# Optimization experiments

Hardware: AMD Instinct MI355X
Metric: run time of the kernel (lower is better)

Reference implementation:

```python
import jax, jax.numpy as jnp
import numpy as np

DIM = 1024
DIM_HEAD = 64
HEADS = 16
INNER = DIM_HEAD * HEADS  # 1024
B, N1, N2 = 8, 4096, 256
EPS = 1e-5


def layer_norm(x, w, b):
    mu = jnp.mean(x, axis=-1, keepdims=True)
    var = jnp.var(x, axis=-1, keepdims=True)
    return (x - mu) * jax.lax.rsqrt(var + EPS) * w + b


def setup_inputs() -> dict:
    key = jax.random.key(0)
    ks = jax.random.split(key, 10)
    return {
        "x": jax.random.normal(ks[0], (B, N1, DIM), jnp.float32),
        "latents": jax.random.normal(ks[1], (B, N2, DIM), jnp.float32),
        "shift": jax.random.normal(ks[2], (B, DIM), jnp.float32),
        "scale": jax.random.normal(ks[3], (B, DIM), jnp.float32),
        "ln1_w": jnp.ones((DIM,), jnp.float32),
        "ln1_b": jnp.zeros((DIM,), jnp.float32),
        "ln2_w": jnp.ones((DIM,), jnp.float32),
        "ln2_b": jnp.zeros((DIM,), jnp.float32),
        "Wq": jax.random.normal(ks[4], (INNER, DIM), jnp.float32) * 0.02,
        "Wkv": jax.random.normal(ks[5], (2 * INNER, DIM), jnp.float32) * 0.02,
        "Wo": jax.random.normal(ks[6], (DIM, INNER), jnp.float32) * 0.02,
    }


def reference(x, latents, shift, scale, ln1_w, ln1_b, ln2_w, ln2_b, Wq, Wkv, Wo):
    x = layer_norm(x, ln1_w, ln1_b)                      # (b, n1, D)
    lat = layer_norm(latents, ln2_w, ln2_b)              # (b, n2, D)
    lat = lat * (1.0 + scale[:, None, :]) + shift[:, None, :]

    b, n2, _ = lat.shape
    q = jnp.einsum('bld,ed->ble', lat, Wq)               # (b, n2, inner)
    kv_in = jnp.concatenate((x, lat), axis=-2)           # (b, n1+n2, D)
    kv = jnp.einsum('bld,ed->ble', kv_in, Wkv)           # (b, n1+n2, 2*inner)
    k, v = jnp.split(kv, 2, axis=-1)

    def to_heads(t):
        bsz, L, _ = t.shape
        return t.reshape(bsz, L, HEADS, DIM_HEAD).transpose(0, 2, 1, 3)

    q, k, v = to_heads(q), to_heads(k), to_heads(v)      # (b, h, L, dh)
    attn_scale = 1.0 / np.sqrt(np.sqrt(DIM_HEAD)).astype(np.float32)
    logits = jnp.einsum('bhqd,bhkd->bhqk', q * attn_scale, k * attn_scale)
    w = jax.nn.softmax(logits.astype(jnp.float32), axis=-1).astype(logits.dtype)
    out = jnp.einsum('bhqk,bhkd->bhqd', w, v)            # (b, h, n2, dh)
    out = out.transpose(0, 2, 1, 3).reshape(b, n2, INNER)
    return jnp.einsum('ble,de->bld', out, Wo)            # (b, n2, D)
```

## Files before the change

### kernel.cpp

```cpp
#include <hip/hip_runtime.h>
#include <cstdint>
#include <cstddef>

#define B_SZ 8
#define N1 4096
#define N2 256
#define LTOT 4352
#define DIMD 1024
#define HEADS 16
#define DH 64
#define MKV (B_SZ * LTOT)

typedef _Float16 f16;
typedef f16 f16x4_t __attribute__((ext_vector_type(4)));
typedef f16 f16x8_t __attribute__((ext_vector_type(8)));
typedef float f32x4_t __attribute__((ext_vector_type(4)));

__device__ __forceinline__ void g2l16(const void* g, void* l) {
  __builtin_amdgcn_global_load_lds(
      (__attribute__((address_space(1))) void*)g,
      (__attribute__((address_space(3))) void*)l, 16, 0, 0);
}

__global__ __launch_bounds__(256) void ln_mod_kernel(
    const float* __restrict__ x, const float* __restrict__ lat,
    const float* __restrict__ shift, const float* __restrict__ scale,
    const float* __restrict__ ln1w, const float* __restrict__ ln1b,
    const float* __restrict__ ln2w, const float* __restrict__ ln2b,
    f16* __restrict__ kv_in) {
  const int row = blockIdx.x;
  const int b = row / LTOT;
  const int n = row - b * LTOT;
  const int tid = threadIdx.x;
  const bool is_lat = (n >= N1);
  const float* src = is_lat ? (lat + (size_t)(b * N2 + (n - N1)) * DIMD)
                            : (x + (size_t)(b * N1 + n) * DIMD);
  float4 v = ((const float4*)src)[tid];
  float s = v.x + v.y + v.z + v.w;
  float s2 = v.x * v.x + v.y * v.y + v.z * v.z + v.w * v.w;
#pragma unroll
  for (int m = 1; m <= 32; m <<= 1) {
    s += __shfl_xor(s, m, 64);
    s2 += __shfl_xor(s2, m, 64);
  }
  __shared__ float red[8];
  const int wave = tid >> 6;
  if ((tid & 63) == 0) { red[wave * 2] = s; red[wave * 2 + 1] = s2; }
  __syncthreads();
  s = red[0] + red[2] + red[4] + red[6];
  s2 = red[1] + red[3] + red[5] + red[7];
  const float mean = s * (1.0f / DIMD);
  const float var = fmaxf(s2 * (1.0f / DIMD) - mean * mean, 0.0f);
  const float rstd = rsqrtf(var + 1e-5f);
  const float4 w4 = ((const float4*)(is_lat ? ln2w : ln1w))[tid];
  const float4 b4 = ((const float4*)(is_lat ? ln2b : ln1b))[tid];
  float y0 = (v.x - mean) * rstd * w4.x + b4.x;
  float y1 = (v.y - mean) * rstd * w4.y + b4.y;
  float y2 = (v.z - mean) * rstd * w4.z + b4.z;
  float y3 = (v.w - mean) * rstd * w4.w + b4.w;
  if (is_lat) {
    float4 sc = ((const float4*)(scale + (size_t)b * DIMD))[tid];
    float4 sh = ((const float4*)(shift + (size_t)b * DIMD))[tid];
    y0 = y0 * (1.0f + sc.x) + sh.x;
    y1 = y1 * (1.0f + sc.y) + sh.y;
    y2 = y2 * (1.0f + sc.z) + sh.z;
    y3 = y3 * (1.0f + sc.w) + sh.w;
  }
  f16x4_t o = {(f16)y0, (f16)y1, (f16)y2, (f16)y3};
  *(f16x4_t*)(kv_in + (size_t)row * DIMD + tid * 4) = o;
}

__global__ __launch_bounds__(256) void cast_kernel(const float* __restrict__ in,
                                                   f16* __restrict__ out, int n4) {
  const int i = blockIdx.x * 256 + threadIdx.x;
  if (i < n4) {
    float4 v = ((const float4*)in)[i];
    f16x4_t o = {(f16)v.x, (f16)v.y, (f16)v.z, (f16)v.w};
    ((f16x4_t*)out)[i] = o;
  }
}

template <int MODE>
__global__ __launch_bounds__(256) void gemm128(
    const f16* __restrict__ A0, const f16* __restrict__ BT,
    void* __restrict__ out0, void* __restrict__ out1) {
  const int mt = blockIdx.x, nt = blockIdx.y;
  const f16* Abase;
  if (MODE == 1) {
    const int bb = mt >> 1;
    Abase = A0 + ((size_t)(bb * LTOT + N1 + (mt & 1) * 128)) * DIMD;
  } else {
    Abase = A0 + (size_t)mt * 128 * DIMD;
  }
  const f16* Bbase = BT + (size_t)nt * 128 * DIMD;
  __shared__ alignas(16) f16 As[128 * 32];
  __shared__ alignas(16) f16 Bs[128 * 32];
  const int tid = threadIdx.x;
  const int wave = tid >> 6, lane = tid & 63;
  const int wm = (wave & 1) * 64, wn = (wave >> 1) * 64;
  const int lrow = lane >> 2, lcol = (lane & 3) * 8;
  const int r16 = lane & 15, g8 = (lane >> 4) * 8, q4 = (lane >> 4) * 4;
  f32x4_t acc[4][4] = {};
  for (int k0 = 0; k0 < DIMD; k0 += 32) {
    __syncthreads();
    g2l16(Abase + (size_t)(wave * 16 + lrow) * DIMD + k0 + lcol, &As[(wave * 16) * 32]);
    g2l16(Abase + (size_t)(64 + wave * 16 + lrow) * DIMD + k0 + lcol, &As[(64 + wave * 16) * 32]);
    g2l16(Bbase + (size_t)(wave * 16 + lrow) * DIMD + k0 + lcol, &Bs[(wave * 16) * 32]);
    g2l16(Bbase + (size_t)(64 + wave * 16 + lrow) * DIMD + k0 + lcol, &Bs[(64 + wave * 16) * 32]);
    __syncthreads();
    f16x8_t a[4], bf[4];
#pragma unroll
    for (int i = 0; i < 4; i++)
      a[i] = *(const f16x8_t*)&As[(wm + i * 16 + r16) * 32 + g8];
#pragma unroll
    for (int j = 0; j < 4; j++)
      bf[j] = *(const f16x8_t*)&Bs[(wn + j * 16 + r16) * 32 + g8];
#pragma unroll
    for (int i = 0; i < 4; i++)
#pragma unroll
      for (int j = 0; j < 4; j++)
        acc[i][j] = __builtin_amdgcn_mfma_f32_16x16x32_f16(a[i], bf[j], acc[i][j], 0, 0, 0);
  }

  if constexpr (MODE == 0) {
    const int m0 = mt * 128;
    const int b = m0 / LTOT;
    const int n0 = m0 - b * LTOT;
    const int e0 = nt * 128;
    if (e0 < 1024) {
      f16* kbuf = (f16*)out0;
#pragma unroll
      for (int i = 0; i < 4; i++) {
        const int n_base = n0 + wm + i * 16 + q4;
#pragma unroll
        for (int j = 0; j < 4; j++) {
          const int e = e0 + wn + j * 16 + r16;
          const int h = e >> 6, d = e & 63;
          const size_t base = ((size_t)(b * HEADS + h) * LTOT);
#pragma unroll
          for (int r = 0; r < 4; r++)
            kbuf[(base + n_base + r) * DH + d] = (f16)acc[i][j][r];
        }
      }
    } else {
      f16* vbuf = (f16*)out1;
      const int e0v = e0 - 1024;
#pragma unroll
      for (int i = 0; i < 4; i++) {
        const int n_base = n0 + wm + i * 16 + q4;
#pragma unroll
        for (int j = 0; j < 4; j++) {
          const int e = e0v + wn + j * 16 + r16;
          const int h = e >> 6, d = e & 63;
          f16x4_t pk = {(f16)acc[i][j][0], (f16)acc[i][j][1],
                        (f16)acc[i][j][2], (f16)acc[i][j][3]};
          *(f16x4_t*)&vbuf[((size_t)(b * HEADS + h) * DH + d) * LTOT + n_base] = pk;
        }
      }
    }
  } else if constexpr (MODE == 1) {
    f16* qbuf = (f16*)out0;
    const int b = mt >> 1;
#pragma unroll
    for (int i = 0; i < 4; i++) {
      const int n_base = (mt & 1) * 128 + wm + i * 16 + q4;
#pragma unroll
      for (int j = 0; j < 4; j++) {
        const int e = nt * 128 + wn + j * 16 + r16;
        const int h = e >> 6, d = e & 63;
#pragma unroll
        for (int r = 0; r < 4; r++)
          qbuf[((size_t)(b * HEADS + h) * N2 + n_base + r) * DH + d] = (f16)acc[i][j][r];
      }
    }
  } else {
    float* outp = (float*)out0;
    const int m0 = mt * 128;
#pragma unroll
    for (int i = 0; i < 4; i++) {
#pragma unroll
      for (int j = 0; j < 4; j++) {
        const int col = nt * 128 + wn + j * 16 + r16;
#pragma unroll
        for (int r = 0; r < 4; r++)
          outp[(size_t)(m0 + wm + i * 16 + q4 + r) * DIMD + col] = acc[i][j][r];
      }
    }
  }
}

__global__ __launch_bounds__(256, 1) void attn_kernel(
    const f16* __restrict__ qbuf, const f16* __restrict__ kbuf,
    const f16* __restrict__ vbuf, f16* __restrict__ attn_out) {
  const int bh = blockIdx.x >> 1;
  const int qt = blockIdx.x & 1;
  const int b = bh >> 4, h = bh & 15;
  const f16* qg = qbuf + ((size_t)bh * N2 + qt * 128) * DH;
  const f16* kg = kbuf + (size_t)bh * LTOT * DH;
  const f16* vg = vbuf + (size_t)bh * DH * LTOT;

  __shared__ alignas(16) f16 Rh[17408];
  __shared__ alignas(16) f16 Vs[4][64 * 32];

  const int tid = threadIdx.x, wave = tid >> 6, lane = tid & 63;
  const int lrow = lane >> 2, lcol = (lane & 3) * 8;
  const int r16 = lane & 15, g8 = (lane >> 4) * 8, q4 = (lane >> 4) * 4;
  f16* Ps = &Rh[wave * 4352];

#pragma unroll
  for (int s = 0; s < 2; s++)
#pragma unroll
    for (int half = 0; half < 2; half++) {
      const int r0 = half * 64 + wave * 16;
      g2l16(qg + (size_t)(r0 + lrow) * DH + s * 32 + lcol,
            &Rh[8192 + s * 4096 + r0 * 32]);
    }
  __syncthreads();
  f16x8_t bQ[2][2];
#pragma unroll
  for (int s = 0; s < 2; s++)
#pragma unroll
    for (int j = 0; j < 2; j++)
      bQ[s][j] = *(const f16x8_t*)&Rh[8192 + s * 4096 + (wave * 32 + j * 16 + r16) * 32 + g8];

  f32x4_t oacc[4][2] = {};
  float mrow[2] = {-1e30f, -1e30f};
  float lsum[2] = {0.0f, 0.0f};
  const float SCL = 0.125f * 1.44269504089f;

  for (int kt = 0; kt < LTOT / 128; kt++) {
    __syncthreads();
#pragma unroll
    for (int s = 0; s < 2; s++)
#pragma unroll
      for (int half = 0; half < 2; half++) {
        const int r0 = half * 64 + wave * 16;
        g2l16(kg + (size_t)(kt * 128 + r0 + lrow) * DH + s * 32 + lcol,
              &Rh[s * 4096 + r0 * 32]);
      }
#pragma unroll
    for (int dg = 0; dg < 4; dg++) {
      const int d0 = dg * 16;
      g2l16(vg + (size_t)(d0 + lrow) * LTOT + kt * 128 + wave * 32 + lcol,
            &Vs[wave][d0 * 32]);
    }
    __syncthreads();
    f32x4_t sacc[8][2] = {};
#pragma unroll
    for (int s = 0; s < 2; s++) {
      f16x8_t aK[8];
#pragma unroll
      for (int i = 0; i < 8; i++)
        aK[i] = *(const f16x8_t*)&Rh[s * 4096 + (i * 16 + r16) * 32 + g8];
#pragma unroll
      for (int i = 0; i < 8; i++)
#pragma unroll
        for (int j = 0; j < 2; j++)
          sacc[i][j] = __builtin_amdgcn_mfma_f32_16x16x32_f16(aK[i], bQ[s][j], sacc[i][j], 0, 0, 0);
    }
    __syncthreads();
#pragma unroll
    for (int j = 0; j < 2; j++) {
      float vmax = -1e30f;
#pragma unroll
      for (int i = 0; i < 8; i++)
#pragma unroll
        for (int r = 0; r < 4; r++) vmax = fmaxf(vmax, sacc[i][j][r]);
      vmax = fmaxf(vmax, __shfl_xor(vmax, 16, 64));
      vmax = fmaxf(vmax, __shfl_xor(vmax, 32, 64));
      const float m_new = fmaxf(mrow[j], SCL * vmax);
      const float alpha = exp2f(mrow[j] - m_new);
      float psum = 0.0f;
#pragma unroll
      for (int i = 0; i < 8; i++) {
        f16x4_t pk;
#pragma unroll
        for (int r = 0; r < 4; r++) {
          const float p = exp2f(SCL * sacc[i][j][r] - m_new);
          psum += p;
          pk[r] = (f16)p;
        }
        *(f16x4_t*)&Ps[(j * 16 + r16) * 136 + i * 16 + q4] = pk;
      }
      psum += __shfl_xor(psum, 16, 64);
      psum += __shfl_xor(psum, 32, 64);
      lsum[j] = lsum[j] * alpha + psum;
      mrow[j] = m_new;
#pragma unroll
      for (int id = 0; id < 4; id++) oacc[id][j] *= alpha;
    }
#pragma unroll
    for (int s2 = 0; s2 < 4; s2++) {
      f16x8_t aV[4];
#pragma unroll
      for (int id = 0; id < 4; id++)
        aV[id] = *(const f16x8_t*)&Vs[s2][(id * 16 + r16) * 32 + g8];
      f16x8_t bP[2];
#pragma unroll
      for (int j = 0; j < 2; j++)
        bP[j] = *(const f16x8_t*)&Ps[(j * 16 + r16) * 136 + s2 * 32 + g8];
#pragma unroll
      for (int id = 0; id < 4; id++)
#pragma unroll
        for (int j = 0; j < 2; j++)
          oacc[id][j] = __builtin_amdgcn_mfma_f32_16x16x32_f16(aV[id], bP[j], oacc[id][j], 0, 0, 0);
    }
  }
#pragma unroll
  for (int j = 0; j < 2; j++) {
    const float inv = 1.0f / lsum[j];
    const int qrow = qt * 128 + wave * 32 + j * 16 + r16;
    const size_t rowbase = ((size_t)(b * N2 + qrow)) * DIMD + h * DH;
#pragma unroll
    for (int id = 0; id < 4; id++) {
      f16x4_t pk;
#pragma unroll
      for (int r = 0; r < 4; r++) pk[r] = (f16)(oacc[id][j][r] * inv);
      *(f16x4_t*)&attn_out[rowbase + id * 16 + q4] = pk;
    }
  }
}

extern "C" void kernel_launch(void* const* d_in, const int* in_sizes, int n_in,
                              void* d_out, int out_size, void* d_ws, size_t ws_size,
                              hipStream_t stream) {
  const float* x     = (const float*)d_in[0];
  const float* lat   = (const float*)d_in[1];
  const float* shift = (const float*)d_in[2];
  const float* scale = (const float*)d_in[3];
  const float* ln1w  = (const float*)d_in[4];
  const float* ln1b  = (const float*)d_in[5];
  const float* ln2w  = (const float*)d_in[6];
  const float* ln2b  = (const float*)d_in[7];
  const float* Wq    = (const float*)d_in[8];
  const float* Wkv   = (const float*)d_in[9];
  const float* Wo    = (const float*)d_in[10];
  float* outp = (float*)d_out;

  char* ws = (char*)d_ws;
  f16* kv_in = (f16*)ws;                 ws += (size_t)MKV * DIMD * 2;
  f16* Wq16  = (f16*)ws;                 ws += (size_t)1024 * 1024 * 2;
  f16* Wkv16 = (f16*)ws;                 ws += (size_t)2048 * 1024 * 2;
  f16* Wo16  = (f16*)ws;                 ws += (size_t)1024 * 1024 * 2;
  f16* qbuf  = (f16*)ws;                 ws += (size_t)B_SZ * HEADS * N2 * DH * 2;
  f16* kbuf  = (f16*)ws;                 ws += (size_t)B_SZ * HEADS * LTOT * DH * 2;
  f16* vbuf  = (f16*)ws;                 ws += (size_t)B_SZ * HEADS * LTOT * DH * 2;
  f16* aout  = (f16*)ws;                 ws += (size_t)B_SZ * N2 * DIMD * 2;

  ln_mod_kernel<<<dim3(MKV), dim3(256), 0, stream>>>(x, lat, shift, scale, ln1w,
                                                     ln1b, ln2w, ln2b, kv_in);
  cast_kernel<<<dim3(1024), dim3(256), 0, stream>>>(Wq, Wq16, 1024 * 1024 / 4);
  cast_kernel<<<dim3(2048), dim3(256), 0, stream>>>(Wkv, Wkv16, 2048 * 1024 / 4);
  cast_kernel<<<dim3(1024), dim3(256), 0, stream>>>(Wo, Wo16, 1024 * 1024 / 4);

  gemm128<0><<<dim3(MKV / 128, 16), dim3(256), 0, stream>>>(kv_in, Wkv16, kbuf, vbuf);
  gemm128<1><<<dim3(16, 8), dim3(256), 0, stream>>>(kv_in, Wq16, qbuf, nullptr);
  attn_kernel<<<dim3(256), dim3(256), 0, stream>>>(qbuf, kbuf, vbuf, aout);
  gemm128<2><<<dim3(16, 8), dim3(256), 0, stream>>>(aout, Wo16, outp, nullptr);
}
```

Before: 594.0 us.

## Split attention over key dimension with separate merge kernel

Each (batch, head, query tile) attention block is split into two halves along the key sequence. Each half writes unnormalized fp32 partial outputs plus row max and sum into reused workspace, and a new merge kernel combines them with log-sum-exp weights into fp16 output. This doubles the grid to give more blocks per CU for latency hiding. The cost is extra global traffic for partials and an additional kernel launch.

```diff
diff --git a/kernel.cpp b/kernel.cpp
--- a/kernel.cpp
+++ b/kernel.cpp
@@ -10,6 +10,9 @@
 #define HEADS 16
 #define DH 64
 #define MKV (B_SZ * LTOT)
+#define KSPLIT 2
+#define KTILES (LTOT / 128)
+#define KT_PER (KTILES / KSPLIT)
 
 typedef _Float16 f16;
 typedef f16 f16x4_t __attribute__((ext_vector_type(4)));
@@ -191,10 +194,12 @@
 
 __global__ __launch_bounds__(256, 1) void attn_kernel(
     const f16* __restrict__ qbuf, const f16* __restrict__ kbuf,
-    const f16* __restrict__ vbuf, f16* __restrict__ attn_out) {
-  const int bh = blockIdx.x >> 1;
-  const int qt = blockIdx.x & 1;
-  const int b = bh >> 4, h = bh & 15;
+    const f16* __restrict__ vbuf, float* __restrict__ Op,
+    float* __restrict__ ml) {
+  const int part = blockIdx.x;
+  const int bh = part >> 2;
+  const int qt = (part >> 1) & 1;
+  const int ks = part & 1;
   const f16* qg = qbuf + ((size_t)bh * N2 + qt * 128) * DH;
   const f16* kg = kbuf + (size_t)bh * LTOT * DH;
   const f16* vg = vbuf + (size_t)bh * DH * LTOT;
@@ -228,7 +233,7 @@
   float lsum[2] = {0.0f, 0.0f};
   const float SCL = 0.125f * 1.44269504089f;
 
-  for (int kt = 0; kt < LTOT / 128; kt++) {
+  for (int kt = ks * KT_PER; kt < ks * KT_PER + KT_PER; kt++) {
     __syncthreads();
 #pragma unroll
     for (int s = 0; s < 2; s++)
@@ -306,18 +311,52 @@
           oacc[id][j] = __builtin_amdgcn_mfma_f32_16x16x32_f16(aV[id], bP[j], oacc[id][j], 0, 0, 0);
     }
   }
+  float* Opb = Op + (size_t)part * 128 * 64;
 #pragma unroll
   for (int j = 0; j < 2; j++) {
-    const float inv = 1.0f / lsum[j];
-    const int qrow = qt * 128 + wave * 32 + j * 16 + r16;
-    const size_t rowbase = ((size_t)(b * N2 + qrow)) * DIMD + h * DH;
-#pragma unroll
-    for (int id = 0; id < 4; id++) {
-      f16x4_t pk;
-#pragma unroll
-      for (int r = 0; r < 4; r++) pk[r] = (f16)(oacc[id][j][r] * inv);
-      *(f16x4_t*)&attn_out[rowbase + id * 16 + q4] = pk;
-    }
+    const int q_local = wave * 32 + j * 16 + r16;
+#pragma unroll
+    for (int id = 0; id < 4; id++)
+      *(float4*)&Opb[(size_t)q_local * 64 + id * 16 + q4] = *(float4*)&oacc[id][j];
+    if (lane < 16) {
+      const size_t mi = ((size_t)part * 128 + wave * 32 + j * 16 + lane) * 2;
+      ml[mi] = mrow[j];
+      ml[mi + 1] = lsum[j];
+    }
+  }
+}
+
+__global__ __launch_bounds__(256) void attn_merge_kernel(
+    const float* __restrict__ Op, const float* __restrict__ ml,
+    f16* __restrict__ aout) {
+  const int bq = blockIdx.x;
+  const int bh = bq >> 1, qt = bq & 1;
+  const int b = bh >> 4, h = bh & 15;
+  const int tid = threadIdx.x;
+  __shared__ float w0s[128], w1s[128];
+  if (tid < 128) {
+    const size_t i0 = ((size_t)(bq * 2 + 0) * 128 + tid) * 2;
+    const size_t i1 = ((size_t)(bq * 2 + 1) * 128 + tid) * 2;
+    const float m0 = ml[i0], l0 = ml[i0 + 1];
+    const float m1 = ml[i1], l1 = ml[i1 + 1];
+    const float M = fmaxf(m0, m1);
+    const float w0 = exp2f(m0 - M), w1 = exp2f(m1 - M);
+    const float invL = 1.0f / (l0 * w0 + l1 * w1);
+    w0s[tid] = w0 * invL;
+    w1s[tid] = w1 * invL;
+  }
+  __syncthreads();
+  const float4* O0 = (const float4*)(Op + (size_t)(bq * 2 + 0) * 128 * 64);
+  const float4* O1 = (const float4*)(Op + (size_t)(bq * 2 + 1) * 128 * 64);
+#pragma unroll
+  for (int p = 0; p < 8; p++) {
+    const int idx = p * 256 + tid;
+    const int q = idx >> 4, c = idx & 15;
+    const float4 a = O0[idx], bb = O1[idx];
+    const float w0 = w0s[q], w1 = w1s[q];
+    f16x4_t o = {(f16)(a.x * w0 + bb.x * w1), (f16)(a.y * w0 + bb.y * w1),
+                 (f16)(a.z * w0 + bb.z * w1), (f16)(a.w * w0 + bb.w * w1)};
+    *(f16x4_t*)&aout[((size_t)(b * N2 + qt * 128 + q)) * DIMD + h * DH + c * 4] = o;
   }
 }
 
@@ -347,6 +386,9 @@
   f16* vbuf  = (f16*)ws;                 ws += (size_t)B_SZ * HEADS * LTOT * DH * 2;
   f16* aout  = (f16*)ws;                 ws += (size_t)B_SZ * N2 * DIMD * 2;
 
+  float* Opart = (float*)kv_in;
+  float* mlbuf = (float*)(kv_in + (size_t)512 * 128 * 64 * 2);
+
   ln_mod_kernel<<<dim3(MKV), dim3(256), 0, stream>>>(x, lat, shift, scale, ln1w,
                                                      ln1b, ln2w, ln2b, kv_in);
   cast_kernel<<<dim3(1024), dim3(256), 0, stream>>>(Wq, Wq16, 1024 * 1024 / 4);
@@ -355,6 +397,8 @@
 
   gemm128<0><<<dim3(MKV / 128, 16), dim3(256), 0, stream>>>(kv_in, Wkv16, kbuf, vbuf);
   gemm128<1><<<dim3(16, 8), dim3(256), 0, stream>>>(kv_in, Wq16, qbuf, nullptr);
-  attn_kernel<<<dim3(256), dim3(256), 0, stream>>>(qbuf, kbuf, vbuf, aout);
+  attn_kernel<<<dim3(128 * 2 * KSPLIT), dim3(256), 0, stream>>>(qbuf, kbuf, vbuf,
+                                                                Opart, mlbuf);
+  attn_merge_kernel<<<dim3(256), dim3(256), 0, stream>>>(Opart, mlbuf, aout);
   gemm128<2><<<dim3(16, 8), dim3(256), 0, stream>>>(aout, Wo16, outp, nullptr);
 }
```

Result: slower. 611.9 us (+3.0%).
